# Optimization experiments

Measured on AMD Instinct MI355X. Metric: run time of the kernel, lower is better.

Reference implementation:

```python
import jax, jax.numpy as jnp
import numpy as np

N = 50000      # nodes
E = 800000     # edges
IN = 64        # in_channels
HID = 256      # hidden_dim
LAT = 64       # latent_dim
KS = 2         # kernel_size per dim
DIM = 3        # pseudo-coordinate dim
K = KS ** DIM  # 8 spline weight matrices


def spline_basis_coeffs(pseudo, ks, dim, dtype):
    """Degree-1 open B-spline basis: returns per-edge coefficients c [E, ks**dim]."""
    e = pseudo.shape[0]
    v = pseudo * (ks - 1)                                   # [E, dim]
    bot = jnp.clip(jnp.floor(v), 0, ks - 1).astype(jnp.int32)
    frac = v - bot
    c = jnp.zeros((e, ks ** dim), dtype)
    rows = jnp.arange(e)
    for s in range(2 ** dim):  # 8 knot combinations (fixed small loop)
        w = jnp.ones(e, dtype)
        idx = jnp.zeros(e, jnp.int32)
        for d in range(dim):
            bit = (s >> d) & 1
            w = w * (frac[:, d] if bit else 1.0 - frac[:, d])
            idx = idx + jnp.clip(bot[:, d] + bit, 0, ks - 1) * (ks ** d)
        c = c.at[rows, idx].add(w)
    return c


def spline_conv(x, edge_index, pseudo, W, Wroot, b):
    """SplineConv with aggr='mean', root weight and bias (degree-1 open splines)."""
    src, dst = edge_index[0], edge_index[1]
    n = x.shape[0]
    e = pseudo.shape[0]
    c = spline_basis_coeffs(pseudo, KS, DIM, x.dtype)        # [E, K]
    x_src = x[src]                                           # [E, in] gather
    deg = jax.ops.segment_sum(jnp.ones(e, x.dtype), dst, num_segments=n)
    inv_deg = (1.0 / jnp.maximum(deg, 1.0))[:, None]         # [N, 1] mean aggr
    out = jnp.zeros((n, W.shape[2]), x.dtype)
    for k in range(W.shape[0]):  # K=8 fixed loop; scatter-add then dense matmul
        agg = jax.ops.segment_sum(c[:, k:k + 1] * x_src, dst, num_segments=n)
        out = out + (agg * inv_deg) @ W[k]
    return out + x @ Wroot + b


def setup_inputs() -> dict:
    key = jax.random.key(0)
    ks = jax.random.split(key, 12)
    x = jax.random.normal(ks[0], (N, IN), jnp.float32)
    edge_index = jax.random.randint(ks[1], (2, E), 0, N, jnp.int32)
    s = 0.05
    return {
        "x": x,
        "edge_index": edge_index,
        "conv1_W": jax.random.normal(ks[2], (K, IN, HID), jnp.float32) * s,
        "conv1_root": jax.random.normal(ks[3], (IN, HID), jnp.float32) * s,
        "conv1_b": jnp.zeros((HID,), jnp.float32),
        "conv2_W": jax.random.normal(ks[4], (K, HID, LAT), jnp.float32) * s,
        "conv2_root": jax.random.normal(ks[5], (HID, LAT), jnp.float32) * s,
        "conv2_b": jnp.zeros((LAT,), jnp.float32),
        "dec_w1": jax.random.normal(ks[6], (LAT, HID), jnp.float32) * s,
        "dec_b1": jnp.zeros((HID,), jnp.float32),
        "dec_w2": jax.random.normal(ks[7], (HID, IN), jnp.float32) * s,
        "dec_b2": jnp.zeros((IN,), jnp.float32),
    }


def reference(x, edge_index, conv1_W, conv1_root, conv1_b,
              conv2_W, conv2_root, conv2_b,
              dec_w1, dec_b1, dec_w2, dec_b2):
    pseudo = jnp.zeros((edge_index.shape[1], DIM), x.dtype)  # forward builds zeros
    h = jax.nn.relu(spline_conv(x, edge_index, pseudo, conv1_W, conv1_root, conv1_b))
    z = spline_conv(h, edge_index, pseudo, conv2_W, conv2_root, conv2_b)
    h2 = jax.nn.relu(z @ dec_w1 + dec_b1)
    return h2 @ dec_w2 + dec_b2
```

## Files before the change

### kernel.cpp

```cpp
#include <hip/hip_runtime.h>
#include <hip/hip_bf16.h>


#define THREADS 256

typedef __attribute__((ext_vector_type(8))) short bf16x8;
typedef __attribute__((ext_vector_type(4))) float f32x4;

__device__ __forceinline__ float bf2f(unsigned short u) {
    unsigned v = ((unsigned)u) << 16;
    return __builtin_bit_cast(float, v);
}
__device__ __forceinline__ unsigned short f2bf(float f) {
    __hip_bfloat16 h = __float2bfloat16(f);
    return __builtin_bit_cast(unsigned short, h);
}
__device__ __forceinline__ void acc4(float* f, uint2 v) {
    f[0] += bf2f((unsigned short)v.x);
    f[1] += bf2f((unsigned short)(v.x >> 16));
    f[2] += bf2f((unsigned short)v.y);
    f[3] += bf2f((unsigned short)(v.y >> 16));
}

__device__ __forceinline__ void pack_one(unsigned short* dst,
                                         const float* W0, const float* W1,
                                         int NB, int ksplit, int colsplit,
                                         int ld0, int ld1, int t) {
    int i = t & 7, lane = (t >> 3) & 63, rest = t >> 9;
    int j = rest % NB, s = rest / NB;
    int k = s * 32 + ((lane >> 4) << 3) + i;
    int c = (j << 4) + (lane & 15);
    float v;
    if (c >= colsplit)    v = W1[(size_t)k * ld1 + (c - colsplit)];
    else if (k >= ksplit) v = W1[(size_t)(k - ksplit) * ld1 + c];
    else                  v = W0[(size_t)k * ld0 + c];
    dst[t] = f2bf(v);
}

#define BIG (1 << 30)

__global__ void prep_kernel(const float* __restrict__ W1g, const float* __restrict__ root1,
                            const float* __restrict__ W2g, const float* __restrict__ root2,
                            const float* __restrict__ dw1, const float* __restrict__ dw2,
                            const float* __restrict__ x, const int* __restrict__ dstv,
                            int* __restrict__ bcnt,
                            unsigned short* __restrict__ Pb1,
                            unsigned short* __restrict__ Pb2,
                            unsigned short* __restrict__ Pd1,
                            unsigned short* __restrict__ Pd2,
                            unsigned short* __restrict__ ab1,
                            int n, int E, int pb_pack) {
    if ((int)blockIdx.x >= pb_pack) {
        __shared__ int hist[256];
        int t = threadIdx.x;
        hist[t] = 0;
        __syncthreads();
        int e0 = ((int)blockIdx.x - pb_pack) * 4096;
#pragma unroll
        for (int i = 0; i < 16; ++i) {
            int e = e0 + t + i * 256;
            if (e < E) atomicAdd(&hist[dstv[e] >> 8], 1);
        }
        __syncthreads();
        int h = hist[t];
        if (h) atomicAdd(&bcnt[t], h);
        return;
    }
    int t = blockIdx.x * blockDim.x + threadIdx.x;
    if (t < 32768) {
        pack_one(Pb1, W1g, root1, 16, 64, BIG, 256, 256, t);
    } else if (t < 65536) {
        pack_one(Pb2, W2g, root2, 8, BIG, 64, 64, 64, t - 32768);
    } else if (t < 81920) {
        pack_one(Pd1, dw1, dw1, 16, BIG, BIG, 256, 256, t - 65536);
    } else if (t < 98304) {
        pack_one(Pd2, dw2, dw2, 4, BIG, BIG, 64, 64, t - 81920);
    } else if (t < 98304 + n * 16) {
        int u = t - 98304;
        int row = u >> 4, c4 = (u & 15) * 4;
        float4 v = *(const float4*)(x + (size_t)row * 64 + c4);
        unsigned lo = (unsigned)f2bf(v.x) | ((unsigned)f2bf(v.y) << 16);
        unsigned hi = (unsigned)f2bf(v.z) | ((unsigned)f2bf(v.w) << 16);
        uint2 o; o.x = lo; o.y = hi;
        *(uint2*)(ab1 + (size_t)row * 128 + 64 + c4) = o;
    }
}

__global__ __launch_bounds__(256) void partition_edges(
    const int* __restrict__ src, const int* __restrict__ dst,
    const int* __restrict__ bcnt, int* __restrict__ bcur,
    int* __restrict__ epack, int E) {
    __shared__ int hist[256];
    __shared__ int base[256];
    __shared__ int lcur[256];
    __shared__ int bb[256];
    int t = threadIdx.x;
    hist[t] = 0;
    __syncthreads();
    int e0 = blockIdx.x * 4096;
    int myd[16], mys[16];
#pragma unroll
    for (int i = 0; i < 16; ++i) {
        int e = e0 + t + i * 256;
        int d = (e < E) ? dst[e] : -1;
        mys[i] = (e < E) ? src[e] : 0;
        myd[i] = d;
        if (d >= 0) atomicAdd(&hist[d >> 8], 1);
    }
    int cb = bcnt[t];
    bb[t] = cb;
    __syncthreads();
    for (int off = 1; off < 256; off <<= 1) {
        int xv = (t >= off) ? bb[t - off] : 0;
        __syncthreads();
        bb[t] += xv;
        __syncthreads();
    }
    int bbase_t = bb[t] - cb;
    int h = hist[t];
    if (h > 0) base[t] = bbase_t + atomicAdd(&bcur[t], h);
    lcur[t] = 0;
    __syncthreads();
#pragma unroll
    for (int i = 0; i < 16; ++i) {
        int d = myd[i];
        if (d >= 0) {
            int b = d >> 8;
            int p = atomicAdd(&lcur[b], 1);
            epack[base[b] + p] = ((d & 255) << 20) | mys[i];
        }
    }
}

__global__ __launch_bounds__(256) void bucket_fill2(
    const int* __restrict__ epack, const int* __restrict__ bcnt,
    int* __restrict__ offs, float* __restrict__ invd,
    int* __restrict__ esrc, int N) {
    __shared__ int sb_[256];
    __shared__ int nh[256];
    __shared__ int loff[256];
    __shared__ int ncur[256];
    __shared__ int stage[8192];
    int b = blockIdx.x, t = threadIdx.x;
    int n0 = b << 8;
    int cntn = min(256, N - n0);
    int cb = bcnt[t];
    sb_[t] = cb;
    __syncthreads();
    for (int off = 1; off < 256; off <<= 1) {
        int xv = (t >= off) ? sb_[t - off] : 0;
        __syncthreads();
        sb_[t] += xv;
        __syncthreads();
    }
    int ebase = b ? sb_[b - 1] : 0;
    int ecount = sb_[b] - ebase;
    if (b == 0 && t == 0) offs[N] = sb_[255];
    nh[t] = 0;
    __syncthreads();
    for (int i = t; i < ecount; i += 256)
        atomicAdd(&nh[epack[ebase + i] >> 20], 1);
    __syncthreads();
    int v = nh[t];
    loff[t] = v;
    __syncthreads();
    for (int off = 1; off < 256; off <<= 1) {
        int xv = (t >= off) ? loff[t - off] : 0;
        __syncthreads();
        loff[t] += xv;
        __syncthreads();
    }
    int ex = loff[t] - v;
    loff[t] = ex;
    if (t < cntn) {
        offs[n0 + t] = ebase + ex;
        invd[n0 + t] = 1.0f / (float)max(v, 1);
    }
    ncur[t] = 0;
    __syncthreads();
    bool useLds = (ecount <= 8192);
    for (int i = t; i < ecount; i += 256) {
        int p = epack[ebase + i];
        int dl = p >> 20;
        int pos = atomicAdd(&ncur[dl], 1);
        int g = loff[dl] + pos;
        int sv = p & 0xFFFFF;
        if (useLds) stage[g] = sv;
        else        esrc[ebase + g] = sv;
    }
    __syncthreads();
    if (useLds)
        for (int i = t; i < ecount; i += 256) esrc[ebase + i] = stage[i];
}

__global__ void agg_x4(unsigned short* __restrict__ ab1, const int* __restrict__ esrc,
                       const int* __restrict__ offs, const float* __restrict__ invd,
                       int n) {
    int node = blockIdx.x * 4 + (threadIdx.x >> 6);
    if (node >= n) return;
    int l = threadIdx.x & 63;
    int slot = l >> 4, c = l & 15;
    const unsigned short* xb = ab1 + 64 + c * 4;
    int s = offs[node], e = offs[node + 1];
    float a0[4] = {}, a1[4] = {}, a2[4] = {}, a3[4] = {};
    int j = s;
    for (; j + 16 <= e; j += 16) {
        int i0 = esrc[j + slot],      i1 = esrc[j + 4 + slot];
        int i2 = esrc[j + 8 + slot],  i3 = esrc[j + 12 + slot];
        uint2 v0 = *(const uint2*)(xb + (size_t)i0 * 128);
        uint2 v1 = *(const uint2*)(xb + (size_t)i1 * 128);
        uint2 v2 = *(const uint2*)(xb + (size_t)i2 * 128);
        uint2 v3 = *(const uint2*)(xb + (size_t)i3 * 128);
        acc4(a0, v0); acc4(a1, v1); acc4(a2, v2); acc4(a3, v3);
    }
    for (; j + 4 <= e; j += 4) {
        int i0 = esrc[j + slot];
        uint2 v0 = *(const uint2*)(xb + (size_t)i0 * 128);
        acc4(a0, v0);
    }
    int rem = e - j;
    if (slot < rem) {
        int i0 = esrc[j + slot];
        uint2 v0 = *(const uint2*)(xb + (size_t)i0 * 128);
        acc4(a1, v0);
    }
    float r[4];
#pragma unroll
    for (int k = 0; k < 4; ++k) {
        r[k] = (a0[k] + a1[k]) + (a2[k] + a3[k]);
        r[k] += __shfl_xor(r[k], 16);
        r[k] += __shfl_xor(r[k], 32);
    }
    if (slot == 0) {
        float iv = invd[node];
        unsigned lo = (unsigned)f2bf(r[0] * iv) | ((unsigned)f2bf(r[1] * iv) << 16);
        unsigned hi = (unsigned)f2bf(r[2] * iv) | ((unsigned)f2bf(r[3] * iv) << 16);
        uint2 o; o.x = lo; o.y = hi;
        *(uint2*)(ab1 + (size_t)node * 128 + c * 4) = o;
    }
}

__global__ void agg_z4(const unsigned short* __restrict__ hwroot,
                       const int* __restrict__ esrc, const int* __restrict__ offs,
                       const float* __restrict__ invd, const float* __restrict__ b2,
                       unsigned short* __restrict__ z, int n) {
    int node = blockIdx.x * 4 + (threadIdx.x >> 6);
    if (node >= n) return;
    int l = threadIdx.x & 63;
    int slot = l >> 4, c = l & 15;
    const unsigned short* hb = hwroot + c * 4;
    int s = offs[node], e = offs[node + 1];
    float a0[4] = {}, a1[4] = {}, a2[4] = {}, a3[4] = {};
    int j = s;
    for (; j + 16 <= e; j += 16) {
        int i0 = esrc[j + slot],      i1 = esrc[j + 4 + slot];
        int i2 = esrc[j + 8 + slot],  i3 = esrc[j + 12 + slot];
        uint2 v0 = *(const uint2*)(hb + (size_t)i0 * 128);
        uint2 v1 = *(const uint2*)(hb + (size_t)i1 * 128);
        uint2 v2 = *(const uint2*)(hb + (size_t)i2 * 128);
        uint2 v3 = *(const uint2*)(hb + (size_t)i3 * 128);
        acc4(a0, v0); acc4(a1, v1); acc4(a2, v2); acc4(a3, v3);
    }
    for (; j + 4 <= e; j += 4) {
        int i0 = esrc[j + slot];
        uint2 v0 = *(const uint2*)(hb + (size_t)i0 * 128);
        acc4(a0, v0);
    }
    int rem = e - j;
    if (slot < rem) {
        int i0 = esrc[j + slot];
        uint2 v0 = *(const uint2*)(hb + (size_t)i0 * 128);
        acc4(a1, v0);
    }
    float r[4];
#pragma unroll
    for (int k = 0; k < 4; ++k) {
        r[k] = (a0[k] + a1[k]) + (a2[k] + a3[k]);
        r[k] += __shfl_xor(r[k], 16);
        r[k] += __shfl_xor(r[k], 32);
    }
    if (slot == 0) {
        float iv = invd[node];
        uint2 hr = *(const uint2*)(hwroot + (size_t)node * 128 + 64 + c * 4);
        float v0 = r[0] * iv + bf2f((unsigned short)hr.x) + b2[c * 4 + 0];
        float v1 = r[1] * iv + bf2f((unsigned short)(hr.x >> 16)) + b2[c * 4 + 1];
        float v2 = r[2] * iv + bf2f((unsigned short)hr.y) + b2[c * 4 + 2];
        float v3 = r[3] * iv + bf2f((unsigned short)(hr.y >> 16)) + b2[c * 4 + 3];
        unsigned lo = (unsigned)f2bf(v0) | ((unsigned)f2bf(v1) << 16);
        unsigned hi = (unsigned)f2bf(v2) | ((unsigned)f2bf(v3) << 16);
        uint2 o; o.x = lo; o.y = hi;
        *(uint2*)(z + (size_t)node * 64 + c * 4) = o;
    }
}

template <int K1, int NBW2, bool OUTBF>
__global__ __launch_bounds__(256) void gemm_fused(
    const unsigned short* __restrict__ A,
    const unsigned short* __restrict__ Bp1, const float* __restrict__ bias1,
    const unsigned short* __restrict__ Bp2, const float* __restrict__ bias2,
    void* __restrict__ Cv, int n)
{
    constexpr int KS1 = K1 / 32;
    constexpr int N2 = NBW2 * 64;
    constexpr int NB2 = NBW2 * 4;
    __shared__ unsigned short ht[64][264];

    const int m0 = blockIdx.x * 64;
    const int lane = threadIdx.x & 63;
    const int w = threadIdx.x >> 6;
    const int quad = lane >> 4;
    const int l16 = lane & 15;

    {
        f32x4 acc[4][4] = {};
        const unsigned short* Arow = A + (size_t)(m0 + l16) * K1 + quad * 8;
        for (int s = 0; s < KS1; ++s) {
            bf16x8 a[4];
#pragma unroll
            for (int mb = 0; mb < 4; ++mb)
                a[mb] = *(const bf16x8*)(Arow + (size_t)mb * 16 * K1 + s * 32);
#pragma unroll
            for (int jn = 0; jn < 4; ++jn) {
                int j = w * 4 + jn;
                bf16x8 b = *(const bf16x8*)(Bp1 + ((size_t)(s * 16 + j) * 64 + lane) * 8);
#pragma unroll
                for (int mb = 0; mb < 4; ++mb)
                    acc[mb][jn] = __builtin_amdgcn_mfma_f32_16x16x32_bf16(a[mb], b, acc[mb][jn], 0, 0, 0);
            }
        }
#pragma unroll
        for (int jn = 0; jn < 4; ++jn) {
            int col = (w * 4 + jn) * 16 + l16;
            float bv = bias1[col];
#pragma unroll
            for (int mb = 0; mb < 4; ++mb)
#pragma unroll
                for (int r = 0; r < 4; ++r) {
                    int row = mb * 16 + quad * 4 + r;
                    ht[row][col] = f2bf(fmaxf(acc[mb][jn][r] + bv, 0.f));
                }
        }
    }
    __syncthreads();

    {
        f32x4 acc[4][NBW2] = {};
        for (int s = 0; s < 8; ++s) {
            bf16x8 a[4];
#pragma unroll
            for (int mb = 0; mb < 4; ++mb)
                a[mb] = *(const bf16x8*)&ht[mb * 16 + l16][s * 32 + quad * 8];
#pragma unroll
            for (int jn = 0; jn < NBW2; ++jn) {
                int j = w * NBW2 + jn;
                bf16x8 b = *(const bf16x8*)(Bp2 + ((size_t)(s * NB2 + j) * 64 + lane) * 8);
#pragma unroll
                for (int mb = 0; mb < 4; ++mb)
                    acc[mb][jn] = __builtin_amdgcn_mfma_f32_16x16x32_bf16(a[mb], b, acc[mb][jn], 0, 0, 0);
            }
        }
#pragma unroll
        for (int jn = 0; jn < NBW2; ++jn) {
            int col = (w * NBW2 + jn) * 16 + l16;
            float bv = bias2 ? bias2[col] : 0.f;
#pragma unroll
            for (int mb = 0; mb < 4; ++mb)
#pragma unroll
                for (int r = 0; r < 4; ++r) {
                    int row = m0 + mb * 16 + quad * 4 + r;
                    if (row < n) {
                        float v = acc[mb][jn][r] + bv;
                        if (OUTBF)
                            ((unsigned short*)Cv)[(size_t)row * N2 + col] = f2bf(v);
                        else
                            ((float*)Cv)[(size_t)row * N2 + col] = v;
                    }
                }
        }
    }
}

extern "C" void kernel_launch(void* const* d_in, const int* in_sizes, int n_in,
                              void* d_out, int out_size, void* d_ws, size_t ws_size,
                              hipStream_t stream) {
    const float* x      = (const float*)d_in[0];
    const int*   ei     = (const int*)d_in[1];
    const float* W1g    = (const float*)d_in[2];
    const float* root1  = (const float*)d_in[3];
    const float* b1     = (const float*)d_in[4];
    const float* W2g    = (const float*)d_in[5];
    const float* root2  = (const float*)d_in[6];
    const float* b2     = (const float*)d_in[7];
    const float* dw1    = (const float*)d_in[8];
    const float* db1    = (const float*)d_in[9];
    const float* dw2    = (const float*)d_in[10];
    const float* db2    = (const float*)d_in[11];
    float* out = (float*)d_out;

    const int N = in_sizes[0] / 64;
    const int E = in_sizes[1] / 2;
    const int Npad = N + 64;
    const int* srcv = ei;
    const int* dstv = ei + E;

    char* ws = (char*)d_ws;
    auto alloc = [&](size_t bytes) -> void* {
        void* p = (void*)ws;
        ws += (bytes + 255) & ~(size_t)255;
        return p;
    };
    int*   bcnt   = (int*)alloc(1024);
    int*   bcur   = (int*)alloc(1024);
    int*   offs   = (int*)alloc((size_t)(N + 1) * 4);
    float* invd   = (float*)alloc((size_t)N * 4);
    int*   esrc   = (int*)alloc((size_t)E * 4);
    int*   epack  = (int*)alloc((size_t)E * 4);
    unsigned short* Pb1 = (unsigned short*)alloc(32768 * 2);
    unsigned short* Pb2 = (unsigned short*)alloc(32768 * 2);
    unsigned short* Pd1 = (unsigned short*)alloc(16384 * 2);
    unsigned short* Pd2 = (unsigned short*)alloc(16384 * 2);
    unsigned short* ab1    = (unsigned short*)alloc((size_t)Npad * 128 * 2);
    unsigned short* hwroot = (unsigned short*)alloc((size_t)Npad * 128 * 2);
    unsigned short* z      = (unsigned short*)alloc((size_t)Npad * 64 * 2);

    hipMemsetAsync(bcnt, 0, 2048, stream);

    int gb = (N + 63) / 64;
    int nbkt = (N + 255) / 256;
    int pa = (E + 4095) / 4096;
    int pb_pack = (98304 + N * 16 + THREADS - 1) / THREADS;

    prep_kernel<<<pb_pack + pa, THREADS, 0, stream>>>(
        W1g, root1, W2g, root2, dw1, dw2, x, dstv, bcnt,
        Pb1, Pb2, Pd1, Pd2, ab1, N, E, pb_pack);
    partition_edges<<<pa, 256, 0, stream>>>(srcv, dstv, bcnt, bcur, epack, E);
    bucket_fill2<<<nbkt, 256, 0, stream>>>(epack, bcnt, offs, invd, esrc, N);

    agg_x4<<<(N + 3) / 4, THREADS, 0, stream>>>(ab1, esrc, offs, invd, N);
    gemm_fused<128, 2, true><<<gb, 256, 0, stream>>>(ab1, Pb1, b1, Pb2, nullptr, hwroot, N);
    agg_z4<<<(N + 3) / 4, THREADS, 0, stream>>>(hwroot, esrc, offs, invd, b2, z, N);
    gemm_fused<64, 1, false><<<gb, 256, 0, stream>>>(z, Pd1, db1, Pd2, db2, out, N);
}
```

Baseline: 208.6 us.

## Fuse neighbor aggregation into GEMM kernels, staging aggregated rows in LDS

```diff
diff --git a/kernel.cpp b/kernel.cpp
--- a/kernel.cpp
+++ b/kernel.cpp
@@ -20,6 +20,38 @@
     f[1] += bf2f((unsigned short)(v.x >> 16));
     f[2] += bf2f((unsigned short)v.y);
     f[3] += bf2f((unsigned short)(v.y >> 16));
+}
+
+__device__ __forceinline__ void gather_node(
+    const unsigned short* __restrict__ tab, int rs,
+    const int* __restrict__ esrc, int s, int e, int slot, float* r)
+{
+    float a0[4] = {}, a1[4] = {}, a2[4] = {}, a3[4] = {};
+    int j = s;
+    for (; j + 16 <= e; j += 16) {
+        int i0 = esrc[j + slot],      i1 = esrc[j + 4 + slot];
+        int i2 = esrc[j + 8 + slot],  i3 = esrc[j + 12 + slot];
+        uint2 v0 = *(const uint2*)(tab + (size_t)i0 * rs);
+        uint2 v1 = *(const uint2*)(tab + (size_t)i1 * rs);
+        uint2 v2 = *(const uint2*)(tab + (size_t)i2 * rs);
+        uint2 v3 = *(const uint2*)(tab + (size_t)i3 * rs);
+        acc4(a0, v0); acc4(a1, v1); acc4(a2, v2); acc4(a3, v3);
+    }
+    for (; j + 4 <= e; j += 4) {
+        uint2 v0 = *(const uint2*)(tab + (size_t)esrc[j + slot] * rs);
+        acc4(a0, v0);
+    }
+    if (slot < e - j) {
+        uint2 v0 = *(const uint2*)(tab + (size_t)esrc[j + slot] * rs);
+        acc4(a1, v0);
+    }
+#pragma unroll
+    for (int k = 0; k < 4; ++k) {
+        float v = (a0[k] + a1[k]) + (a2[k] + a3[k]);
+        v += __shfl_xor(v, 16);
+        v += __shfl_xor(v, 32);
+        r[k] = v;
+    }
 }
 
 __device__ __forceinline__ void pack_one(unsigned short* dst,
@@ -48,7 +80,7 @@
                             unsigned short* __restrict__ Pb2,
                             unsigned short* __restrict__ Pd1,
                             unsigned short* __restrict__ Pd2,
-                            unsigned short* __restrict__ ab1,
+                            unsigned short* __restrict__ xb,
                             int n, int E, int pb_pack) {
     if ((int)blockIdx.x >= pb_pack) {
         __shared__ int hist[256];
@@ -82,7 +114,7 @@
         unsigned lo = (unsigned)f2bf(v.x) | ((unsigned)f2bf(v.y) << 16);
         unsigned hi = (unsigned)f2bf(v.z) | ((unsigned)f2bf(v.w) << 16);
         uint2 o; o.x = lo; o.y = hi;
-        *(uint2*)(ab1 + (size_t)row * 128 + 64 + c4) = o;
+        *(uint2*)(xb + (size_t)row * 64 + c4) = o;
     }
 }
 
@@ -193,136 +225,57 @@
         for (int i = t; i < ecount; i += 256) esrc[ebase + i] = stage[i];
 }
 
-__global__ void agg_x4(unsigned short* __restrict__ ab1, const int* __restrict__ esrc,
-                       const int* __restrict__ offs, const float* __restrict__ invd,
-                       int n) {
-    int node = blockIdx.x * 4 + (threadIdx.x >> 6);
-    if (node >= n) return;
-    int l = threadIdx.x & 63;
-    int slot = l >> 4, c = l & 15;
-    const unsigned short* xb = ab1 + 64 + c * 4;
-    int s = offs[node], e = offs[node + 1];
-    float a0[4] = {}, a1[4] = {}, a2[4] = {}, a3[4] = {};
-    int j = s;
-    for (; j + 16 <= e; j += 16) {
-        int i0 = esrc[j + slot],      i1 = esrc[j + 4 + slot];
-        int i2 = esrc[j + 8 + slot],  i3 = esrc[j + 12 + slot];
-        uint2 v0 = *(const uint2*)(xb + (size_t)i0 * 128);
-        uint2 v1 = *(const uint2*)(xb + (size_t)i1 * 128);
-        uint2 v2 = *(const uint2*)(xb + (size_t)i2 * 128);
-        uint2 v3 = *(const uint2*)(xb + (size_t)i3 * 128);
-        acc4(a0, v0); acc4(a1, v1); acc4(a2, v2); acc4(a3, v3);
-    }
-    for (; j + 4 <= e; j += 4) {
-        int i0 = esrc[j + slot];
-        uint2 v0 = *(const uint2*)(xb + (size_t)i0 * 128);
-        acc4(a0, v0);
-    }
-    int rem = e - j;
-    if (slot < rem) {
-        int i0 = esrc[j + slot];
-        uint2 v0 = *(const uint2*)(xb + (size_t)i0 * 128);
-        acc4(a1, v0);
-    }
-    float r[4];
-#pragma unroll
-    for (int k = 0; k < 4; ++k) {
-        r[k] = (a0[k] + a1[k]) + (a2[k] + a3[k]);
-        r[k] += __shfl_xor(r[k], 16);
-        r[k] += __shfl_xor(r[k], 32);
-    }
-    if (slot == 0) {
-        float iv = invd[node];
-        unsigned lo = (unsigned)f2bf(r[0] * iv) | ((unsigned)f2bf(r[1] * iv) << 16);
-        unsigned hi = (unsigned)f2bf(r[2] * iv) | ((unsigned)f2bf(r[3] * iv) << 16);
-        uint2 o; o.x = lo; o.y = hi;
-        *(uint2*)(ab1 + (size_t)node * 128 + c * 4) = o;
-    }
-}
-
-__global__ void agg_z4(const unsigned short* __restrict__ hwroot,
-                       const int* __restrict__ esrc, const int* __restrict__ offs,
-                       const float* __restrict__ invd, const float* __restrict__ b2,
-                       unsigned short* __restrict__ z, int n) {
-    int node = blockIdx.x * 4 + (threadIdx.x >> 6);
-    if (node >= n) return;
-    int l = threadIdx.x & 63;
-    int slot = l >> 4, c = l & 15;
-    const unsigned short* hb = hwroot + c * 4;
-    int s = offs[node], e = offs[node + 1];
-    float a0[4] = {}, a1[4] = {}, a2[4] = {}, a3[4] = {};
-    int j = s;
-    for (; j + 16 <= e; j += 16) {
-        int i0 = esrc[j + slot],      i1 = esrc[j + 4 + slot];
-        int i2 = esrc[j + 8 + slot],  i3 = esrc[j + 12 + slot];
-        uint2 v0 = *(const uint2*)(hb + (size_t)i0 * 128);
-        uint2 v1 = *(const uint2*)(hb + (size_t)i1 * 128);
-        uint2 v2 = *(const uint2*)(hb + (size_t)i2 * 128);
-        uint2 v3 = *(const uint2*)(hb + (size_t)i3 * 128);
-        acc4(a0, v0); acc4(a1, v1); acc4(a2, v2); acc4(a3, v3);
-    }
-    for (; j + 4 <= e; j += 4) {
-        int i0 = esrc[j + slot];
-        uint2 v0 = *(const uint2*)(hb + (size_t)i0 * 128);
-        acc4(a0, v0);
-    }
-    int rem = e - j;
-    if (slot < rem) {
-        int i0 = esrc[j + slot];
-        uint2 v0 = *(const uint2*)(hb + (size_t)i0 * 128);
-        acc4(a1, v0);
-    }
-    float r[4];
-#pragma unroll
-    for (int k = 0; k < 4; ++k) {
-        r[k] = (a0[k] + a1[k]) + (a2[k] + a3[k]);
-        r[k] += __shfl_xor(r[k], 16);
-        r[k] += __shfl_xor(r[k], 32);
-    }
-    if (slot == 0) {
-        float iv = invd[node];
-        uint2 hr = *(const uint2*)(hwroot + (size_t)node * 128 + 64 + c * 4);
-        float v0 = r[0] * iv + bf2f((unsigned short)hr.x) + b2[c * 4 + 0];
-        float v1 = r[1] * iv + bf2f((unsigned short)(hr.x >> 16)) + b2[c * 4 + 1];
-        float v2 = r[2] * iv + bf2f((unsigned short)hr.y) + b2[c * 4 + 2];
-        float v3 = r[3] * iv + bf2f((unsigned short)(hr.y >> 16)) + b2[c * 4 + 3];
-        unsigned lo = (unsigned)f2bf(v0) | ((unsigned)f2bf(v1) << 16);
-        unsigned hi = (unsigned)f2bf(v2) | ((unsigned)f2bf(v3) << 16);
-        uint2 o; o.x = lo; o.y = hi;
-        *(uint2*)(z + (size_t)node * 64 + c * 4) = o;
-    }
-}
-
-template <int K1, int NBW2, bool OUTBF>
-__global__ __launch_bounds__(256) void gemm_fused(
-    const unsigned short* __restrict__ A,
-    const unsigned short* __restrict__ Bp1, const float* __restrict__ bias1,
-    const unsigned short* __restrict__ Bp2, const float* __restrict__ bias2,
-    void* __restrict__ Cv, int n)
+__global__ __launch_bounds__(256) void fused_l1(
+    const unsigned short* __restrict__ xb,
+    const int* __restrict__ esrc, const int* __restrict__ offs,
+    const float* __restrict__ invd,
+    const unsigned short* __restrict__ Pb1, const float* __restrict__ b1,
+    const unsigned short* __restrict__ Pb2,
+    unsigned short* __restrict__ hwroot, int n)
 {
-    constexpr int KS1 = K1 / 32;
-    constexpr int N2 = NBW2 * 64;
-    constexpr int NB2 = NBW2 * 4;
+    __shared__ unsigned short As[64][136];
     __shared__ unsigned short ht[64][264];
-
     const int m0 = blockIdx.x * 64;
-    const int lane = threadIdx.x & 63;
-    const int w = threadIdx.x >> 6;
-    const int quad = lane >> 4;
-    const int l16 = lane & 15;
+    const int t = threadIdx.x;
+    const int lane = t & 63, w = t >> 6;
+    const int slot = lane >> 4, c = lane & 15;
+    const int quad = slot, l16 = c;
+
+#pragma unroll 1
+    for (int i = 0; i < 16; ++i) {
+        int row = w * 16 + i;
+        int node = m0 + row;
+        float r[4] = {0.f, 0.f, 0.f, 0.f};
+        if (node < n)
+            gather_node(xb + c * 4, 64, esrc, offs[node], offs[node + 1], slot, r);
+        if (slot == 0) {
+            float iv = (node < n) ? invd[node] : 0.f;
+            unsigned lo = (unsigned)f2bf(r[0] * iv) | ((unsigned)f2bf(r[1] * iv) << 16);
+            unsigned hi = (unsigned)f2bf(r[2] * iv) | ((unsigned)f2bf(r[3] * iv) << 16);
+            uint2 o; o.x = lo; o.y = hi;
+            *(uint2*)&As[row][c * 4] = o;
+        }
+    }
+    for (int i = t; i < 1024; i += 256) {
+        int row = i >> 4, c4 = (i & 15) * 4;
+        int node = m0 + row;
+        uint2 v; v.x = 0u; v.y = 0u;
+        if (node < n) v = *(const uint2*)(xb + (size_t)node * 64 + c4);
+        *(uint2*)&As[row][64 + c4] = v;
+    }
+    __syncthreads();
 
     {
         f32x4 acc[4][4] = {};
-        const unsigned short* Arow = A + (size_t)(m0 + l16) * K1 + quad * 8;
-        for (int s = 0; s < KS1; ++s) {
+        for (int s = 0; s < 4; ++s) {
             bf16x8 a[4];
 #pragma unroll
             for (int mb = 0; mb < 4; ++mb)
-                a[mb] = *(const bf16x8*)(Arow + (size_t)mb * 16 * K1 + s * 32);
+                a[mb] = *(const bf16x8*)&As[mb * 16 + l16][s * 32 + quad * 8];
 #pragma unroll
             for (int jn = 0; jn < 4; ++jn) {
                 int j = w * 4 + jn;
-                bf16x8 b = *(const bf16x8*)(Bp1 + ((size_t)(s * 16 + j) * 64 + lane) * 8);
+                bf16x8 b = *(const bf16x8*)(Pb1 + ((size_t)(s * 16 + j) * 64 + lane) * 8);
 #pragma unroll
                 for (int mb = 0; mb < 4; ++mb)
                     acc[mb][jn] = __builtin_amdgcn_mfma_f32_16x16x32_bf16(a[mb], b, acc[mb][jn], 0, 0, 0);
@@ -331,7 +284,7 @@
 #pragma unroll
         for (int jn = 0; jn < 4; ++jn) {
             int col = (w * 4 + jn) * 16 + l16;
-            float bv = bias1[col];
+            float bv = b1[col];
 #pragma unroll
             for (int mb = 0; mb < 4; ++mb)
 #pragma unroll
@@ -344,39 +297,129 @@
     __syncthreads();
 
     {
-        f32x4 acc[4][NBW2] = {};
+        f32x4 acc[4][2] = {};
         for (int s = 0; s < 8; ++s) {
             bf16x8 a[4];
 #pragma unroll
             for (int mb = 0; mb < 4; ++mb)
                 a[mb] = *(const bf16x8*)&ht[mb * 16 + l16][s * 32 + quad * 8];
 #pragma unroll
-            for (int jn = 0; jn < NBW2; ++jn) {
-                int j = w * NBW2 + jn;
-                bf16x8 b = *(const bf16x8*)(Bp2 + ((size_t)(s * NB2 + j) * 64 + lane) * 8);
+            for (int jn = 0; jn < 2; ++jn) {
+                int j = w * 2 + jn;
+                bf16x8 b = *(const bf16x8*)(Pb2 + ((size_t)(s * 8 + j) * 64 + lane) * 8);
 #pragma unroll
                 for (int mb = 0; mb < 4; ++mb)
                     acc[mb][jn] = __builtin_amdgcn_mfma_f32_16x16x32_bf16(a[mb], b, acc[mb][jn], 0, 0, 0);
             }
         }
 #pragma unroll
-        for (int jn = 0; jn < NBW2; ++jn) {
-            int col = (w * NBW2 + jn) * 16 + l16;
-            float bv = bias2 ? bias2[col] : 0.f;
+        for (int jn = 0; jn < 2; ++jn) {
+            int col = (w * 2 + jn) * 16 + l16;
 #pragma unroll
             for (int mb = 0; mb < 4; ++mb)
 #pragma unroll
                 for (int r = 0; r < 4; ++r) {
                     int row = m0 + mb * 16 + quad * 4 + r;
-                    if (row < n) {
-                        float v = acc[mb][jn][r] + bv;
-                        if (OUTBF)
-                            ((unsigned short*)Cv)[(size_t)row * N2 + col] = f2bf(v);
-                        else
-                            ((float*)Cv)[(size_t)row * N2 + col] = v;
-                    }
+                    if (row < n)
+                        hwroot[(size_t)row * 128 + col] = f2bf(acc[mb][jn][r]);
                 }
         }
+    }
+}
+
+__global__ __launch_bounds__(256) void fused_dec(
+    const unsigned short* __restrict__ hwroot,
+    const int* __restrict__ esrc, const int* __restrict__ offs,
+    const float* __restrict__ invd, const float* __restrict__ b2,
+    const unsigned short* __restrict__ Pd1, const float* __restrict__ db1,
+    const unsigned short* __restrict__ Pd2, const float* __restrict__ db2,
+    float* __restrict__ out, int n)
+{
+    __shared__ unsigned short Az[64][72];
+    __shared__ unsigned short ht[64][264];
+    const int m0 = blockIdx.x * 64;
+    const int t = threadIdx.x;
+    const int lane = t & 63, w = t >> 6;
+    const int slot = lane >> 4, c = lane & 15;
+    const int quad = slot, l16 = c;
+
+#pragma unroll 1
+    for (int i = 0; i < 16; ++i) {
+        int row = w * 16 + i;
+        int node = m0 + row;
+        float r[4] = {0.f, 0.f, 0.f, 0.f};
+        if (node < n)
+            gather_node(hwroot + c * 4, 128, esrc, offs[node], offs[node + 1], slot, r);
+        if (slot == 0) {
+            uint2 o; o.x = 0u; o.y = 0u;
+            if (node < n) {
+                float iv = invd[node];
+                uint2 hr = *(const uint2*)(hwroot + (size_t)node * 128 + 64 + c * 4);
+                float v0 = r[0] * iv + bf2f((unsigned short)hr.x) + b2[c * 4 + 0];
+                float v1 = r[1] * iv + bf2f((unsigned short)(hr.x >> 16)) + b2[c * 4 + 1];
+                float v2 = r[2] * iv + bf2f((unsigned short)hr.y) + b2[c * 4 + 2];
+                float v3 = r[3] * iv + bf2f((unsigned short)(hr.y >> 16)) + b2[c * 4 + 3];
+                o.x = (unsigned)f2bf(v0) | ((unsigned)f2bf(v1) << 16);
+                o.y = (unsigned)f2bf(v2) | ((unsigned)f2bf(v3) << 16);
+            }
+            *(uint2*)&Az[row][c * 4] = o;
+        }
+    }
+    __syncthreads();
+
+    {
+        f32x4 acc[4][4] = {};
+        for (int s = 0; s < 2; ++s) {
+            bf16x8 a[4];
+#pragma unroll
+            for (int mb = 0; mb < 4; ++mb)
+                a[mb] = *(const bf16x8*)&Az[mb * 16 + l16][s * 32 + quad * 8];
+#pragma unroll
+            for (int jn = 0; jn < 4; ++jn) {
+                int j = w * 4 + jn;
+                bf16x8 b = *(const bf16x8*)(Pd1 + ((size_t)(s * 16 + j) * 64 + lane) * 8);
+#pragma unroll
+                for (int mb = 0; mb < 4; ++mb)
+                    acc[mb][jn] = __builtin_amdgcn_mfma_f32_16x16x32_bf16(a[mb], b, acc[mb][jn], 0, 0, 0);
+            }
+        }
+#pragma unroll
+        for (int jn = 0; jn < 4; ++jn) {
+            int col = (w * 4 + jn) * 16 + l16;
+            float bv = db1[col];
+#pragma unroll
+            for (int mb = 0; mb < 4; ++mb)
+#pragma unroll
+                for (int r = 0; r < 4; ++r) {
+                    int row = mb * 16 + quad * 4 + r;
+                    ht[row][col] = f2bf(fmaxf(acc[mb][jn][r] + bv, 0.f));
+                }
+        }
+    }
+    __syncthreads();
+
+    {
+        f32x4 acc[4] = {};
+        for (int s = 0; s < 8; ++s) {
+            bf16x8 a[4];
+#pragma unroll
+            for (int mb = 0; mb < 4; ++mb)
+                a[mb] = *(const bf16x8*)&ht[mb * 16 + l16][s * 32 + quad * 8];
+            bf16x8 b = *(const bf16x8*)(Pd2 + ((size_t)(s * 4 + w) * 64 + lane) * 8);
+#pragma unroll
+            for (int mb = 0; mb < 4; ++mb)
+                acc[mb] = __builtin_amdgcn_mfma_f32_16x16x32_bf16(a[mb], b, acc[mb], 0, 0, 0);
+        }
+        int col = w * 16 + l16;
+        float bv = db2[col];
+#pragma unroll
+        for (int mb = 0; mb < 4; ++mb)
+#pragma unroll
+            for (int r = 0; r < 4; ++r) {
+                int row = m0 + mb * 16 + quad * 4 + r;
+                if (row < n)
+                    out[(size_t)row * 64 + col] = acc[mb][r] + bv;
+            }
     }
 }
 
@@ -419,9 +462,8 @@
     unsigned short* Pb2 = (unsigned short*)alloc(32768 * 2);
     unsigned short* Pd1 = (unsigned short*)alloc(16384 * 2);
     unsigned short* Pd2 = (unsigned short*)alloc(16384 * 2);
-    unsigned short* ab1    = (unsigned short*)alloc((size_t)Npad * 128 * 2);
+    unsigned short* xb     = (unsigned short*)alloc((size_t)Npad * 64 * 2);
     unsigned short* hwroot = (unsigned short*)alloc((size_t)Npad * 128 * 2);
-    unsigned short* z      = (unsigned short*)alloc((size_t)Npad * 64 * 2);
 
     hipMemsetAsync(bcnt, 0, 2048, stream);
 
@@ -432,12 +474,11 @@
 
     prep_kernel<<<pb_pack + pa, THREADS, 0, stream>>>(
         W1g, root1, W2g, root2, dw1, dw2, x, dstv, bcnt,
-        Pb1, Pb2, Pd1, Pd2, ab1, N, E, pb_pack);
+        Pb1, Pb2, Pd1, Pd2, xb, N, E, pb_pack);
     partition_edges<<<pa, 256, 0, stream>>>(srcv, dstv, bcnt, bcur, epack, E);
     bucket_fill2<<<nbkt, 256, 0, stream>>>(epack, bcnt, offs, invd, esrc, N);
 
-    agg_x4<<<(N + 3) / 4, THREADS, 0, stream>>>(ab1, esrc, offs, invd, N);
-    gemm_fused<128, 2, true><<<gb, 256, 0, stream>>>(ab1, Pb1, b1, Pb2, nullptr, hwroot, N);
-    agg_z4<<<(N + 3) / 4, THREADS, 0, stream>>>(hwroot, esrc, offs, invd, b2, z, N);
-    gemm_fused<64, 1, false><<<gb, 256, 0, stream>>>(z, Pd1, db1, Pd2, db2, out, N);
-}
+    fused_l1<<<gb, 256, 0, stream>>>(xb, esrc, offs, invd, Pb1, b1, Pb2, hwroot, N);
+    fused_dec<<<gb, 256, 0, stream>>>(hwroot, esrc, offs, invd, b2,
+                                      Pd1, db1, Pd2, db2, out, N);
+}
```

Result: slower. 306.4 us (+46.9%).
